# Performance work log

Measured on AMD Instinct MI355X. Metric: run time of the kernel, lower is better.

## Reference

```python
import jax, jax.numpy as jnp
import numpy as np

B, N, F_IN, F_OUT = 8, 2048, 128, 64
ALPHA = 0.2  # LeakyReLU negative slope
NEG_INF = -9e15


def setup_inputs() -> dict:
    key = jax.random.key(0)
    k1, k2, k3, k4 = jax.random.split(key, 4)
    h = jax.random.normal(k1, (B, N, F_IN), dtype=jnp.float32)
    adj = jax.random.randint(k2, (B, N, N), 0, 2, dtype=jnp.int32)
    # xavier_uniform with gain=1.414 approximated by scaled normals (values are arbitrary params)
    W = jax.random.normal(k3, (F_IN, F_OUT), dtype=jnp.float32) * (1.414 * np.sqrt(2.0 / (F_IN + F_OUT)))
    a = jax.random.normal(k4, (2 * F_OUT, 1), dtype=jnp.float32) * (1.414 * np.sqrt(2.0 / (2 * F_OUT + 1)))
    return {"h": h, "adj": adj, "W": W, "a": a}


def reference(h, adj, W, a):
    # Wh: [B, N, F_out]
    Wh = jnp.einsum('bnf,fo->bno', h, W)
    Fo = W.shape[1]
    a1 = a[:Fo, 0]   # [F_out]
    a2 = a[Fo:, 0]   # [F_out]
    # e[b,i,j] = leakyrelu(Wh[b,i]@a1 + Wh[b,j]@a2)  (== cat(Wh_i,Wh_j)@a, same math, no N^2*2F blowup)
    e1 = jnp.einsum('bno,o->bn', Wh, a1)  # [B, N]
    e2 = jnp.einsum('bno,o->bn', Wh, a2)  # [B, N]
    e = e1[:, :, None] + e2[:, None, :]   # [B, N, N]
    e = jnp.where(e > 0, e, ALPHA * e)    # LeakyReLU
    e = jnp.where(adj > 0, e, NEG_INF)    # mask non-edges
    attention = jax.nn.softmax(e, axis=-1)
    # dropout is identity in inference mode (deterministic reference)
    h_prime = jnp.einsum('bij,bjo->bio', attention, Wh)  # [B, N, F_out]
    return jax.nn.elu(h_prime)  # concat=True branch
```

## Files before the change

### kernel.cpp

```cpp
#include <hip/hip_runtime.h>
#include <hip/hip_bf16.h>

#define BB 8
#define NN 2048
#define FIN 128
#define FO 64
#define ALPHA 0.2f

typedef __attribute__((ext_vector_type(8))) short bf16x8;
typedef __attribute__((ext_vector_type(4))) float f32x4;
typedef __attribute__((ext_vector_type(4))) int i32x4;

typedef __attribute__((address_space(1))) const void gvoid;
typedef __attribute__((address_space(3))) void lvoid;

__device__ inline void gl_lds16(const void* g, void* l) {
    __builtin_amdgcn_global_load_lds((gvoid*)g, (lvoid*)l, 16, 0, 0);
}

__device__ inline short f2bf(float x) {
    unsigned u = __float_as_uint(x);
    u += 0x7fffu + ((u >> 16) & 1u);
    return (short)(u >> 16);
}

__global__ __launch_bounds__(256) void wh_kernel(
    const float* __restrict__ h, const float* __restrict__ W,
    const float* __restrict__ a, float* __restrict__ e1, float* __restrict__ e2,
    float* __restrict__ e2p, short* __restrict__ whF)
{
    const int t  = threadIdx.x;
    const int o  = t & 63;
    const int wv = t >> 6;
    const int r0 = blockIdx.x * 32;
    const float* __restrict__ hrow =
        h + (size_t)(r0 + __builtin_amdgcn_readfirstlane(wv) * 8) * FIN;

    float acc[8];
#pragma unroll
    for (int rr = 0; rr < 8; rr++) acc[rr] = 0.f;

    for (int f = 0; f < FIN; f += 4) {
        const float w0 = W[(f + 0) * FO + o];
        const float w1 = W[(f + 1) * FO + o];
        const float w2 = W[(f + 2) * FO + o];
        const float w3 = W[(f + 3) * FO + o];
#pragma unroll
        for (int rr = 0; rr < 8; rr++) {
            const float4 hv = *(const float4*)(hrow + rr * FIN + f);
            acc[rr] = fmaf(hv.x, w0, acc[rr]);
            acc[rr] = fmaf(hv.y, w1, acc[rr]);
            acc[rr] = fmaf(hv.z, w2, acc[rr]);
            acc[rr] = fmaf(hv.w, w3, acc[rr]);
        }
    }

    const int b   = r0 / NN;
    const int ib0 = r0 - b * NN;
    const int ibb = ib0 + wv * 8;
    const int jc  = ibb >> 5;
    const int qq  = (ibb >> 3) & 3;
    const int ot  = o >> 4, mm = o & 15;
    const int L   = mm + qq * 16;
    bf16x8 frag;
#pragma unroll
    for (int rr = 0; rr < 8; rr++) frag[rr] = f2bf(acc[rr]);
    *(bf16x8*)(whF + ((((size_t)(b * 64 + jc) * 4 + ot) * 64 + L) * 8)) = frag;

    const float a1 = a[o], a2 = a[FO + o];
    float vmax = -3.0e38f;
#pragma unroll
    for (int rr = 0; rr < 8; rr++) {
        float v1 = acc[rr] * a1, v2 = acc[rr] * a2;
#pragma unroll
        for (int msk = 32; msk >= 1; msk >>= 1) {
            v1 += __shfl_xor(v1, msk, 64);
            v2 += __shfl_xor(v2, msk, 64);
        }
        vmax = fmaxf(vmax, v2);
        if (o == 0) { e1[r0 + wv * 8 + rr] = v1; e2[r0 + wv * 8 + rr] = v2; }
    }
    if (o == 0) e2p[b * 256 + (ib0 >> 5) * 4 + wv] = vmax;
}

struct SMemS { int adj[16][260]; float e2[256]; };
struct SMemC { float comb[4][16][64]; float lsum[4][16]; };
union __align__(16) SMemU { SMemS s; SMemC c; };

__global__ __launch_bounds__(256, 8) void attn_kernel(
    const int* __restrict__ adj, const float* __restrict__ e1,
    const float* __restrict__ e2, const float* __restrict__ e2p,
    const short* __restrict__ whF, float* __restrict__ pacc,
    float* __restrict__ plsum)
{
    __shared__ SMemU sm;
    __shared__ float red4[4];
    const int t = threadIdx.x, w = t >> 6, lane = t & 63;
    const int m = lane & 15, q = lane >> 4;
    const int blk = blockIdx.x;
    const int jh  = blk >> 10;
    const int tb  = blk & 1023;
    const int b   = tb >> 7;
    const int i0  = (tb & 127) * 16;
    const int i   = i0 + m;

    float pv = e2p[b * 256 + t];
    const float e1v = e1[b * NN + i];
#pragma unroll
    for (int k = 32; k >= 1; k >>= 1) pv = fmaxf(pv, __shfl_xor(pv, k, 64));
    if (lane == 0) red4[w] = pv;
    __syncthreads();
    const float e2mx = fmaxf(fmaxf(red4[0], red4[1]), fmaxf(red4[2], red4[3]));

    float mi = e1v + e2mx;
    mi = mi > 0.f ? mi : ALPHA * mi;

    const short* whFb = whF + (size_t)b * (64 * 4 * 64 * 8);
    const int* arow0 = adj + ((size_t)(b * NN + i0)) * NN + lane * 4;
    const float* e2g = e2 + b * NN + lane * 4;
    const int jbase = jh * 1024;

    f32x4 acc0 = {0.f,0.f,0.f,0.f}, acc1 = acc0, acc2 = acc0, acc3 = acc0;
    float lsum = 0.f;

    for (int tt = 0; tt < 4; tt++) {
        const int j0 = jbase + tt * 256;
#pragma unroll
        for (int k = 0; k < 4; k++) {
            const int r = w * 4 + k;
            gl_lds16(arow0 + (size_t)r * NN + j0, &sm.s.adj[r][0]);
        }
        if (w == 0) gl_lds16(e2g + j0, &sm.s.e2[0]);
        __syncthreads();

#pragma unroll
        for (int s2 = 0; s2 < 2; s2++) {
            const int col = w * 64 + s2 * 32 + q * 8;
            i32x4 a0 = *(const i32x4*)&sm.s.adj[m][col];
            i32x4 a1 = *(const i32x4*)&sm.s.adj[m][col + 4];
            f32x4 ev0 = *(const f32x4*)&sm.s.e2[col];
            f32x4 ev1 = *(const f32x4*)&sm.s.e2[col + 4];

            bf16x8 af;
#pragma unroll
            for (int jj = 0; jj < 8; jj++) {
                const int   av  = (jj < 4) ? a0[jj]      : a1[jj - 4];
                const float e2j = (jj < 4) ? ev0[jj]     : ev1[jj - 4];
                float e = e1v + e2j;
                e = e > 0.f ? e : ALPHA * e;
                const float pe = (av > 0) ? __expf(e - mi) : 0.f;
                lsum += pe;
                af[jj] = f2bf(pe);
            }

            const int jc = (j0 + w * 64 + s2 * 32) >> 5;
            const short* bfp = whFb + (size_t)jc * 2048 + lane * 8;
            bf16x8 b0 = *(const bf16x8*)(bfp);
            bf16x8 b1 = *(const bf16x8*)(bfp + 512);
            bf16x8 b2 = *(const bf16x8*)(bfp + 1024);
            bf16x8 b3 = *(const bf16x8*)(bfp + 1536);

            acc0 = __builtin_amdgcn_mfma_f32_16x16x32_bf16(af, b0, acc0, 0, 0, 0);
            acc1 = __builtin_amdgcn_mfma_f32_16x16x32_bf16(af, b1, acc1, 0, 0, 0);
            acc2 = __builtin_amdgcn_mfma_f32_16x16x32_bf16(af, b2, acc2, 0, 0, 0);
            acc3 = __builtin_amdgcn_mfma_f32_16x16x32_bf16(af, b3, acc3, 0, 0, 0);
        }
        __syncthreads();
    }

    lsum += __shfl_xor(lsum, 16, 64);
    lsum += __shfl_xor(lsum, 32, 64);
    if (q == 0) sm.c.lsum[w][m] = lsum;
#pragma unroll
    for (int ot = 0; ot < 4; ot++) {
        f32x4 av = (ot == 0) ? acc0 : (ot == 1) ? acc1 : (ot == 2) ? acc2 : acc3;
#pragma unroll
        for (int reg = 0; reg < 4; reg++)
            sm.c.comb[w][q * 4 + reg][ot * 16 + m] = av[reg];
    }
    __syncthreads();

    const int row = t >> 4, c0 = (t & 15) * 4;
    f32x4 sum = *(const f32x4*)&sm.c.comb[0][row][c0];
#pragma unroll
    for (int ww = 1; ww < 4; ww++) {
        f32x4 sv = *(const f32x4*)&sm.c.comb[ww][row][c0];
        sum.x += sv.x; sum.y += sv.y; sum.z += sv.z; sum.w += sv.w;
    }
    *(f32x4*)&pacc[((size_t)blk * 16 + row) * 64 + c0] = sum;
    if ((t & 15) == 0) {
        plsum[blk * 16 + row] = sm.c.lsum[0][row] + sm.c.lsum[1][row]
                              + sm.c.lsum[2][row] + sm.c.lsum[3][row];
    }
}

__global__ __launch_bounds__(256) void comb_kernel(
    const float* __restrict__ pacc, const float* __restrict__ plsum,
    float* __restrict__ out)
{
    const int tb = blockIdx.x;
    const int t = threadIdx.x;
    const int row = t >> 4, c0 = (t & 15) * 4;
    const int b = tb >> 7;
    const int i0 = (tb & 127) * 16;

    f32x4 s0 = *(const f32x4*)&pacc[((size_t)tb * 16 + row) * 64 + c0];
    f32x4 s1 = *(const f32x4*)&pacc[((size_t)(1024 + tb) * 16 + row) * 64 + c0];
    float l = plsum[tb * 16 + row] + plsum[(1024 + tb) * 16 + row];
    l = fmaxf(l, 1e-30f);
    const float rl = 1.f / l;
    f32x4 res;
#pragma unroll
    for (int k = 0; k < 4; k++) {
        const float v = (s0[k] + s1[k]) * rl;
        res[k] = v > 0.f ? v : (__expf(v) - 1.f);
    }
    *(f32x4*)&out[((size_t)(b * NN + i0 + row)) * FO + c0] = res;
}

extern "C" void kernel_launch(void* const* d_in, const int* in_sizes, int n_in,
                              void* d_out, int out_size, void* d_ws, size_t ws_size,
                              hipStream_t stream) {
    const float* h   = (const float*)d_in[0];
    const int*   adj = (const int*)d_in[1];
    const float* W   = (const float*)d_in[2];
    const float* a   = (const float*)d_in[3];
    float* out = (float*)d_out;

    char* ws = (char*)d_ws;
    short* whF = (short*)ws;
    size_t off = (size_t)BB * 64 * 4 * 64 * 8 * sizeof(short);
    float* e1  = (float*)(ws + off);  off += (size_t)BB * NN * 4;
    float* e2  = (float*)(ws + off);  off += (size_t)BB * NN * 4;
    float* e2p = (float*)(ws + off);  off += (size_t)BB * 256 * 4;
    float* pacc  = (float*)(ws + off); off += (size_t)2048 * 16 * 64 * 4;
    float* plsum = (float*)(ws + off);

    wh_kernel<<<(BB * NN) / 32, 256, 0, stream>>>(h, W, a, e1, e2, e2p, whF);
    attn_kernel<<<2048, 256, 0, stream>>>(adj, e1, e2, e2p, whF, pacc, plsum);
    comb_kernel<<<1024, 256, 0, stream>>>(pacc, plsum, out);
}
```

Baseline: 257.3 us.

## Drop split-J partials and fuse normalization and ELU into attention kernel

The attention kernel no longer splits the key dimension across two blocks. Each block now walks all 2048 columns in 512-wide LDS tiles and normalizes and applies ELU in place, so the separate combine kernel and the partial accumulator round trip through global memory are gone. The cost is half as many blocks (1024), a doubled LDS footprint, and launch bounds lowered to 4 blocks per CU, which reduces parallelism and latency hiding for the bandwidth-bound adjacency stream.

Measured after the change: 224.8 us. 12.6% less time.

```diff
diff --git a/kernel.cpp b/kernel.cpp
--- a/kernel.cpp
+++ b/kernel.cpp
@@ -83,26 +83,23 @@
     if (o == 0) e2p[b * 256 + (ib0 >> 5) * 4 + wv] = vmax;
 }
 
-struct SMemS { int adj[16][260]; float e2[256]; };
+struct SMemS { int adj[16][516]; float e2[512]; };
 struct SMemC { float comb[4][16][64]; float lsum[4][16]; };
 union __align__(16) SMemU { SMemS s; SMemC c; };
 
-__global__ __launch_bounds__(256, 8) void attn_kernel(
+__global__ __launch_bounds__(256, 4) void attn_kernel(
     const int* __restrict__ adj, const float* __restrict__ e1,
     const float* __restrict__ e2, const float* __restrict__ e2p,
-    const short* __restrict__ whF, float* __restrict__ pacc,
-    float* __restrict__ plsum)
+    const short* __restrict__ whF, float* __restrict__ out)
 {
     __shared__ SMemU sm;
     __shared__ float red4[4];
     const int t = threadIdx.x, w = t >> 6, lane = t & 63;
     const int m = lane & 15, q = lane >> 4;
     const int blk = blockIdx.x;
-    const int jh  = blk >> 10;
-    const int tb  = blk & 1023;
-    const int b   = tb >> 7;
-    const int i0  = (tb & 127) * 16;
-    const int i   = i0 + m;
+    const int b  = blk >> 7;
+    const int i0 = (blk & 127) * 16;
+    const int i  = i0 + m;
 
     float pv = e2p[b * 256 + t];
     const float e1v = e1[b * NN + i];
@@ -116,26 +113,29 @@
     mi = mi > 0.f ? mi : ALPHA * mi;
 
     const short* whFb = whF + (size_t)b * (64 * 4 * 64 * 8);
-    const int* arow0 = adj + ((size_t)(b * NN + i0)) * NN + lane * 4;
+    const int* arow = adj + (size_t)(b * NN + i0 + w * 4) * NN + lane * 4;
     const float* e2g = e2 + b * NN + lane * 4;
-    const int jbase = jh * 1024;
 
     f32x4 acc0 = {0.f,0.f,0.f,0.f}, acc1 = acc0, acc2 = acc0, acc3 = acc0;
     float lsum = 0.f;
 
     for (int tt = 0; tt < 4; tt++) {
-        const int j0 = jbase + tt * 256;
-#pragma unroll
-        for (int k = 0; k < 4; k++) {
-            const int r = w * 4 + k;
-            gl_lds16(arow0 + (size_t)r * NN + j0, &sm.s.adj[r][0]);
-        }
-        if (w == 0) gl_lds16(e2g + j0, &sm.s.e2[0]);
+        const int j0 = tt * 512;
+#pragma unroll
+        for (int rr = 0; rr < 4; rr++) {
+            const int* src = arow + (size_t)rr * NN + j0;
+            gl_lds16(src,        &sm.s.adj[w * 4 + rr][0]);
+            gl_lds16(src + 256,  &sm.s.adj[w * 4 + rr][256]);
+        }
+        if (w == 0) {
+            gl_lds16(e2g + j0,        &sm.s.e2[0]);
+            gl_lds16(e2g + j0 + 256,  &sm.s.e2[256]);
+        }
         __syncthreads();
 
 #pragma unroll
-        for (int s2 = 0; s2 < 2; s2++) {
-            const int col = w * 64 + s2 * 32 + q * 8;
+        for (int s2 = 0; s2 < 4; s2++) {
+            const int col = w * 128 + s2 * 32 + q * 8;
             i32x4 a0 = *(const i32x4*)&sm.s.adj[m][col];
             i32x4 a1 = *(const i32x4*)&sm.s.adj[m][col + 4];
             f32x4 ev0 = *(const f32x4*)&sm.s.e2[col];
@@ -153,7 +153,7 @@
                 af[jj] = f2bf(pe);
             }
 
-            const int jc = (j0 + w * 64 + s2 * 32) >> 5;
+            const int jc = (j0 + w * 128 + s2 * 32) >> 5;
             const short* bfp = whFb + (size_t)jc * 2048 + lane * 8;
             bf16x8 b0 = *(const bf16x8*)(bfp);
             bf16x8 b1 = *(const bf16x8*)(bfp + 512);
@@ -187,34 +187,14 @@
         f32x4 sv = *(const f32x4*)&sm.c.comb[ww][row][c0];
         sum.x += sv.x; sum.y += sv.y; sum.z += sv.z; sum.w += sv.w;
     }
-    *(f32x4*)&pacc[((size_t)blk * 16 + row) * 64 + c0] = sum;
-    if ((t & 15) == 0) {
-        plsum[blk * 16 + row] = sm.c.lsum[0][row] + sm.c.lsum[1][row]
-                              + sm.c.lsum[2][row] + sm.c.lsum[3][row];
-    }
-}
-
-__global__ __launch_bounds__(256) void comb_kernel(
-    const float* __restrict__ pacc, const float* __restrict__ plsum,
-    float* __restrict__ out)
-{
-    const int tb = blockIdx.x;
-    const int t = threadIdx.x;
-    const int row = t >> 4, c0 = (t & 15) * 4;
-    const int b = tb >> 7;
-    const int i0 = (tb & 127) * 16;
-
-    f32x4 s0 = *(const f32x4*)&pacc[((size_t)tb * 16 + row) * 64 + c0];
-    f32x4 s1 = *(const f32x4*)&pacc[((size_t)(1024 + tb) * 16 + row) * 64 + c0];
-    float l = plsum[tb * 16 + row] + plsum[(1024 + tb) * 16 + row];
+    float l = sm.c.lsum[0][row] + sm.c.lsum[1][row] + sm.c.lsum[2][row] + sm.c.lsum[3][row];
     l = fmaxf(l, 1e-30f);
     const float rl = 1.f / l;
+    float vr[4] = { sum.x * rl, sum.y * rl, sum.z * rl, sum.w * rl };
     f32x4 res;
 #pragma unroll
-    for (int k = 0; k < 4; k++) {
-        const float v = (s0[k] + s1[k]) * rl;
-        res[k] = v > 0.f ? v : (__expf(v) - 1.f);
-    }
+    for (int kk = 0; kk < 4; kk++)
+        res[kk] = vr[kk] > 0.f ? vr[kk] : (__expf(vr[kk]) - 1.f);
     *(f32x4*)&out[((size_t)(b * NN + i0 + row)) * FO + c0] = res;
 }
 
@@ -232,11 +212,8 @@
     size_t off = (size_t)BB * 64 * 4 * 64 * 8 * sizeof(short);
     float* e1  = (float*)(ws + off);  off += (size_t)BB * NN * 4;
     float* e2  = (float*)(ws + off);  off += (size_t)BB * NN * 4;
-    float* e2p = (float*)(ws + off);  off += (size_t)BB * 256 * 4;
-    float* pacc  = (float*)(ws + off); off += (size_t)2048 * 16 * 64 * 4;
-    float* plsum = (float*)(ws + off);
+    float* e2p = (float*)(ws + off);
 
     wh_kernel<<<(BB * NN) / 32, 256, 0, stream>>>(h, W, a, e1, e2, e2p, whF);
-    attn_kernel<<<2048, 256, 0, stream>>>(adj, e1, e2, e2p, whF, pacc, plsum);
-    comb_kernel<<<1024, 256, 0, stream>>>(pacc, plsum, out);
-}
+    attn_kernel<<<BB * (NN / 16), 256, 0, stream>>>(adj, e1, e2, e2p, whF, out);
+}
```
